# Kernel tuning notes

Hardware: AMD Instinct MI355X
Metric: run time of the kernel (lower is better)

Reference implementation:

```python
import jax, jax.numpy as jnp
import numpy as np

B, L, D = 16, 2048, 320          # batch, frames, stacked feature dim (80 mel * 4 reduction)
CODEBOOK_SIZE, CODEBOOK_DIM = 8192, 16


def setup_inputs() -> dict:
    key = jax.random.key(0)
    k1, k2, k3 = jax.random.split(key, 3)
    masked_target_values = jax.random.normal(k1, (B, L, D), dtype=jnp.float32)
    # xavier_uniform_ for shape (D, codebook_dim): bound = sqrt(6/(fan_in+fan_out))
    bound = np.sqrt(6.0 / (D + CODEBOOK_DIM)).astype(np.float32)
    project_mat = jax.random.uniform(k2, (D, CODEBOOK_DIM), dtype=jnp.float32,
                                     minval=-bound, maxval=bound)
    cb = jax.random.normal(k3, (CODEBOOK_SIZE, CODEBOOK_DIM), dtype=jnp.float32)
    codebook_norm = cb / jnp.maximum(jnp.linalg.norm(cb, axis=-1, keepdims=True), 1e-12)
    return {"masked_target_values": masked_target_values,
            "project_mat": project_mat,
            "codebook_norm": codebook_norm}


def reference(masked_target_values, project_mat, codebook_norm):
    # project: (B, L, D) @ (D, K) -> (B, L, K)
    targets = jnp.einsum('bld,dk->blk', masked_target_values, project_mat)
    # L2 normalize along last dim (torch F.normalize with eps=1e-12)
    targets_norm = targets / jnp.maximum(
        jnp.linalg.norm(targets, axis=-1, keepdims=True), 1e-12)
    x2 = jnp.sum(targets_norm * targets_norm, axis=-1, keepdims=True)      # (B, L, 1)
    c2 = jnp.sum(codebook_norm * codebook_norm, axis=-1)                   # (C,)
    xc = jnp.einsum('blk,ck->blc', targets_norm, codebook_norm)            # (B, L, C)
    d2 = jnp.maximum(x2 + c2[None, None, :] - 2.0 * xc, 0.0)
    vector_distances = jnp.sqrt(d2)
    labels = jnp.argmin(vector_distances, axis=-1)                         # (B, L) int
    return labels
```

## Files before the change

### kernel.cpp

```cpp
#include <hip/hip_runtime.h>
#include <cfloat>

#define TOKENS 32768
#define DIM    320
#define NCODE  8192
#define NSPLIT 8
#define SPAN   (NCODE / NSPLIT)
#define NTILE  (SPAN / 32)
#define CERT_UNITS 32u
#define FBWAVES 2048

typedef __attribute__((ext_vector_type(8)))  short short8;
typedef __attribute__((ext_vector_type(16))) float f32x16;
typedef unsigned short ushort_t;
typedef unsigned int   uint_t;

static __device__ __forceinline__ ushort_t f2bf(float f) {
    uint_t u = __float_as_uint(f);
    u += 0x7fffu + ((u >> 16) & 1u);
    return (ushort_t)(u >> 16);
}
static __device__ __forceinline__ float bf2f(ushort_t h) {
    return __uint_as_float(((uint_t)h) << 16);
}
static __device__ __forceinline__ uint_t pack2(ushort_t a, ushort_t b) {
    return (uint_t)a | ((uint_t)b << 16);
}
static __device__ __forceinline__ uint_t umaxu(uint_t a, uint_t b) { return a > b ? a : b; }
static __device__ __forceinline__ uint_t uminu(uint_t a, uint_t b) { return a < b ? a : b; }

__global__ __launch_bounds__(128) void prep_kernel(
    const float* __restrict__ x,
    const float* __restrict__ P,
    const float* __restrict__ cb,
    float* __restrict__ tn,
    float* __restrict__ x2o,
    float* __restrict__ c2o,
    ushort_t* __restrict__ tnpack,
    ushort_t* __restrict__ cbpack,
    int* __restrict__ cnt)
{
    __shared__ float Ps[DIM * 16];
    int bid = blockIdx.x, tid = threadIdx.x;
    if (bid < TOKENS / 128) {
        const float4* P4 = (const float4*)P;
        float4* Ps4 = (float4*)Ps;
        #pragma unroll
        for (int i = 0; i < 10; ++i) Ps4[tid + i * 128] = P4[tid + i * 128];
        __syncthreads();

        int tok = bid * 128 + tid;
        const float4* xr = (const float4*)(x + (size_t)tok * DIM);
        float acc[16];
        #pragma unroll
        for (int k = 0; k < 16; ++k) acc[k] = 0.f;
        for (int c = 0; c < 10; ++c) {
            float4 xv[8];
            #pragma unroll
            for (int u = 0; u < 8; ++u) xv[u] = xr[c * 8 + u];
            #pragma unroll
            for (int u = 0; u < 8; ++u) {
                float xs[4] = {xv[u].x, xv[u].y, xv[u].z, xv[u].w};
                #pragma unroll
                for (int e = 0; e < 4; ++e) {
                    int d = c * 32 + u * 4 + e;
                    const float4* pr = (const float4*)(Ps + d * 16);
                    float4 p0 = pr[0], p1 = pr[1], p2 = pr[2], p3 = pr[3];
                    float xe = xs[e];
                    acc[0] = fmaf(xe, p0.x, acc[0]);   acc[1] = fmaf(xe, p0.y, acc[1]);
                    acc[2] = fmaf(xe, p0.z, acc[2]);   acc[3] = fmaf(xe, p0.w, acc[3]);
                    acc[4] = fmaf(xe, p1.x, acc[4]);   acc[5] = fmaf(xe, p1.y, acc[5]);
                    acc[6] = fmaf(xe, p1.z, acc[6]);   acc[7] = fmaf(xe, p1.w, acc[7]);
                    acc[8] = fmaf(xe, p2.x, acc[8]);   acc[9] = fmaf(xe, p2.y, acc[9]);
                    acc[10] = fmaf(xe, p2.z, acc[10]); acc[11] = fmaf(xe, p2.w, acc[11]);
                    acc[12] = fmaf(xe, p3.x, acc[12]); acc[13] = fmaf(xe, p3.y, acc[13]);
                    acc[14] = fmaf(xe, p3.z, acc[14]); acc[15] = fmaf(xe, p3.w, acc[15]);
                }
            }
        }
        float ss = 0.f;
        #pragma unroll
        for (int k = 0; k < 16; ++k) ss = fmaf(acc[k], acc[k], ss);
        float nrm = fmaxf(sqrtf(ss), 1e-12f);
        float t[16];
        #pragma unroll
        for (int k = 0; k < 16; ++k) t[k] = acc[k] / nrm;
        float xx = 0.f;
        #pragma unroll
        for (int k = 0; k < 16; ++k) xx = fmaf(t[k], t[k], xx);

        float4* tf = (float4*)(tn + (size_t)tok * 16);
        tf[0] = make_float4(t[0], t[1], t[2], t[3]);
        tf[1] = make_float4(t[4], t[5], t[6], t[7]);
        tf[2] = make_float4(t[8], t[9], t[10], t[11]);
        tf[3] = make_float4(t[12], t[13], t[14], t[15]);
        x2o[tok] = xx;

        ushort_t hi[16], lo[16];
        #pragma unroll
        for (int k = 0; k < 16; ++k) {
            hi[k] = f2bf(t[k]);
            lo[k] = f2bf(t[k] - bf2f(hi[k]));
        }
        uint4* dst = (uint4*)(tnpack + (size_t)tok * 32);
        dst[0] = make_uint4(pack2(hi[0], hi[1]), pack2(hi[2], hi[3]),
                            pack2(hi[4], hi[5]), pack2(hi[6], hi[7]));
        dst[1] = make_uint4(pack2(hi[8], hi[9]), pack2(hi[10], hi[11]),
                            pack2(hi[12], hi[13]), pack2(hi[14], hi[15]));
        dst[2] = make_uint4(pack2(lo[0], lo[1]), pack2(lo[2], lo[3]),
                            pack2(lo[4], lo[5]), pack2(lo[6], lo[7]));
        dst[3] = make_uint4(pack2(lo[8], lo[9]), pack2(lo[10], lo[11]),
                            pack2(lo[12], lo[13]), pack2(lo[14], lo[15]));
    } else {
        int j = (bid - TOKENS / 128) * 128 + tid;
        const float4* cr4 = (const float4*)(cb + (size_t)j * 16);
        float4 c0 = cr4[0], c1 = cr4[1], c2v = cr4[2], c3 = cr4[3];
        float c[16] = {c0.x, c0.y, c0.z, c0.w, c1.x, c1.y, c1.z, c1.w,
                       c2v.x, c2v.y, c2v.z, c2v.w, c3.x, c3.y, c3.z, c3.w};
        float s = 0.f;
        #pragma unroll
        for (int k = 0; k < 16; ++k) s = fmaf(c[k], c[k], s);
        c2o[j] = s;
        ushort_t hi[16], lo[16];
        #pragma unroll
        for (int k = 0; k < 16; ++k) {
            hi[k] = f2bf(c[k]);
            lo[k] = f2bf(c[k] - bf2f(hi[k]));
        }
        uint4* dst = (uint4*)(cbpack + (size_t)j * 32);
        dst[0] = make_uint4(pack2(hi[0], hi[1]), pack2(hi[2], hi[3]),
                            pack2(hi[4], hi[5]), pack2(hi[6], hi[7]));
        dst[1] = make_uint4(pack2(hi[8], hi[9]), pack2(hi[10], hi[11]),
                            pack2(hi[12], hi[13]), pack2(hi[14], hi[15]));
        dst[2] = make_uint4(pack2(lo[0], lo[1]), pack2(lo[2], lo[3]),
                            pack2(lo[4], lo[5]), pack2(lo[6], lo[7]));
        dst[3] = make_uint4(pack2(lo[8], lo[9]), pack2(lo[10], lo[11]),
                            pack2(lo[12], lo[13]), pack2(lo[14], lo[15]));
        if (j == 0) cnt[0] = 0;
    }
}

__global__ __launch_bounds__(256, 4) void search_kernel(
    const ushort_t* __restrict__ tnpack,
    const ushort_t* __restrict__ cbpack,
    uint_t* __restrict__ pp1,
    uint_t* __restrict__ pp2)
{
    int lane = threadIdx.x & 63;
    int wave = threadIdx.x >> 6;
    int half = lane >> 5;
    int l31  = lane & 31;
    int split = blockIdx.y;
    int tbase = blockIdx.x * 128 + wave * 32;

    const ushort_t* tp = tnpack + (size_t)(tbase + l31) * 32;
    short8 hiA = *(const short8*)(tp + half * 8);
    short8 loA = *(const short8*)(tp + 16 + half * 8);

    f32x16 zero = {};
    uint_t p1[16], p2[16];
    #pragma unroll
    for (int r = 0; r < 16; ++r) { p1[r] = 0u; p2[r] = 0u; }

    for (int t = 0; t < NTILE; ++t) {
        int crow = split * SPAN + t * 32 + l31;
        const ushort_t* cp = cbpack + (size_t)crow * 32;
        short8 hiB = *(const short8*)(cp + half * 8);
        short8 loB = *(const short8*)(cp + 16 + half * 8);

        f32x16 acc = __builtin_amdgcn_mfma_f32_32x32x16_bf16(hiA, hiB, zero, 0, 0, 0);
        acc = __builtin_amdgcn_mfma_f32_32x32x16_bf16(loA, hiB, acc, 0, 0, 0);
        acc = __builtin_amdgcn_mfma_f32_32x32x16_bf16(hiA, loB, acc, 0, 0, 0);

        uint_t inv = 8191u - (uint_t)crow;
        #pragma unroll
        for (int r = 0; r < 16; ++r) {
            float kf = fmaf(acc[r], 131072.0f, 131072.0f);
            uint_t ku = (uint_t)kf;
            uint_t p  = (ku << 13) | inv;
            p2[r] = umaxu(p2[r], uminu(p, p1[r]));
            p1[r] = umaxu(p1[r], p);
        }
    }

    #pragma unroll
    for (int mask = 1; mask <= 16; mask <<= 1) {
        #pragma unroll
        for (int r = 0; r < 16; ++r) {
            uint_t a1 = (uint_t)__shfl_xor((int)p1[r], mask);
            uint_t a2 = (uint_t)__shfl_xor((int)p2[r], mask);
            uint_t np2 = umaxu(uminu(p1[r], a1), umaxu(p2[r], a2));
            p1[r] = umaxu(p1[r], a1);
            p2[r] = np2;
        }
    }

    #pragma unroll
    for (int r = 0; r < 16; ++r) {
        if (l31 == r) {
            int mrow = (r & 3) + 8 * (r >> 2) + 4 * half;
            size_t slot = (size_t)split * TOKENS + (tbase + mrow);
            pp1[slot] = p1[r];
            pp2[slot] = p2[r];
        }
    }
}

__global__ __launch_bounds__(256) void reduce_flag_kernel(
    const uint_t* __restrict__ pp1,
    const uint_t* __restrict__ pp2,
    int* __restrict__ out,
    int* __restrict__ cnt,
    int* __restrict__ flag)
{
    int tok = blockIdx.x * 256 + threadIdx.x;
    uint_t p1 = pp1[tok], p2 = pp2[tok];
    #pragma unroll
    for (int s = 1; s < NSPLIT; ++s) {
        uint_t a1 = pp1[(size_t)s * TOKENS + tok];
        uint_t a2 = pp2[(size_t)s * TOKENS + tok];
        uint_t np2 = umaxu(uminu(p1, a1), umaxu(p2, a2));
        p1 = umaxu(p1, a1);
        p2 = np2;
    }
    out[tok] = 8191 - (int)(p1 & 8191u);
    if ((p1 >> 13) - (p2 >> 13) <= CERT_UNITS) {
        int pz = atomicAdd(cnt, 1);
        flag[pz] = tok;
    }
}

__global__ __launch_bounds__(256) void fallback_kernel(
    const float* __restrict__ tn,
    const float* __restrict__ x2i,
    const float* __restrict__ cb,
    const float* __restrict__ c2i,
    const int* __restrict__ cnt,
    const int* __restrict__ flag,
    int* __restrict__ out)
{
    int lane = threadIdx.x & 63;
    int wid = blockIdx.x * 4 + (threadIdx.x >> 6);
    int n = cnt[0];
    for (int f = wid; f < n; f += FBWAVES) {
        int tok = flag[f];
        const float4* tr = (const float4*)(tn + (size_t)tok * 16);
        float4 t0 = tr[0], t1 = tr[1], t2 = tr[2], t3 = tr[3];
        float a[16] = {t0.x, t0.y, t0.z, t0.w, t1.x, t1.y, t1.z, t1.w,
                       t2.x, t2.y, t2.z, t2.w, t3.x, t3.y, t3.z, t3.w};
        float xx = x2i[tok];
        float mn = FLT_MAX;
        int   id = 0x7fffffff;

        int j = lane;
        const float4* c4p = (const float4*)(cb + (size_t)j * 16);
        float4 n0 = c4p[0], n1 = c4p[1], n2 = c4p[2], n3 = c4p[3];
        float ncc = c2i[j];

        for (int jj = 0; jj < 128; ++jj) {
            float4 c0 = n0, c1 = n1, c2v = n2, c3 = n3;
            float cc = ncc;
            int cj = j;
            j += 64;
            if (jj < 127) {
                const float4* nx = (const float4*)(cb + (size_t)j * 16);
                n0 = nx[0]; n1 = nx[1]; n2 = nx[2]; n3 = nx[3];
                ncc = c2i[j];
            }
            float dot = 0.f;
            dot = fmaf(a[0], c0.x, dot);   dot = fmaf(a[1], c0.y, dot);
            dot = fmaf(a[2], c0.z, dot);   dot = fmaf(a[3], c0.w, dot);
            dot = fmaf(a[4], c1.x, dot);   dot = fmaf(a[5], c1.y, dot);
            dot = fmaf(a[6], c1.z, dot);   dot = fmaf(a[7], c1.w, dot);
            dot = fmaf(a[8], c2v.x, dot);  dot = fmaf(a[9], c2v.y, dot);
            dot = fmaf(a[10], c2v.z, dot); dot = fmaf(a[11], c2v.w, dot);
            dot = fmaf(a[12], c3.x, dot);  dot = fmaf(a[13], c3.y, dot);
            dot = fmaf(a[14], c3.z, dot);  dot = fmaf(a[15], c3.w, dot);
            float e = fmaf(-2.f, dot, xx + cc);
            if (e < mn) { mn = e; id = cj; }
        }
        #pragma unroll
        for (int mask = 1; mask <= 32; mask <<= 1) {
            float pmn = __shfl_xor(mn, mask);
            int   pid = __shfl_xor(id, mask);
            bool take = (pmn < mn) || (pmn == mn && pid < id);
            if (take) { mn = pmn; id = pid; }
        }
        if (lane == 0) out[tok] = id;
    }
}

extern "C" void kernel_launch(void* const* d_in, const int* in_sizes, int n_in,
                              void* d_out, int out_size, void* d_ws, size_t ws_size,
                              hipStream_t stream) {
    const float* x   = (const float*)d_in[0];
    const float* P   = (const float*)d_in[1];
    const float* cbn = (const float*)d_in[2];

    float* ws = (float*)d_ws;
    float*  tn   = ws;
    float*  x2   = tn + (size_t)TOKENS * 16;
    float*  c2   = x2 + TOKENS;
    uint_t* pp1  = (uint_t*)(c2 + NCODE);
    uint_t* pp2  = pp1 + (size_t)NSPLIT * TOKENS;
    int*    flag = (int*)(pp2 + (size_t)NSPLIT * TOKENS);
    int*    cnt  = flag + TOKENS;
    ushort_t* tnpack = (ushort_t*)(cnt + 16);
    ushort_t* cbpack = tnpack + (size_t)TOKENS * 32;
    int* labels = (int*)d_out;

    prep_kernel<<<TOKENS / 128 + NCODE / 128, 128, 0, stream>>>(
        x, P, cbn, tn, x2, c2, tnpack, cbpack, cnt);
    dim3 sg(TOKENS / 128, NSPLIT);
    search_kernel<<<sg, 256, 0, stream>>>(tnpack, cbpack, pp1, pp2);
    reduce_flag_kernel<<<TOKENS / 256, 256, 0, stream>>>(pp1, pp2, labels, cnt, flag);
    fallback_kernel<<<FBWAVES / 4, 256, 0, stream>>>(tn, x2, cbn, c2, cnt, flag, labels);
}
```

Before: 185.0 us.

## Split projection across 8 lanes per token with shuffle reduction

The prep kernel's projection now gives each token 8 lanes. Each lane handles a strided subset of the 320 features and reads x at addresses that coalesce across neighbouring lanes, instead of one thread striding a whole 1280-byte row. Partial sums are combined with xor shuffles, the projection matrix in shared memory is padded to 20-float rows to cut bank conflicts, and the output writes are split across the lanes. This is meant to fix poor memory coalescing and low parallelism (previously only 256 token blocks), at the cost of shuffle work and redundant normalization computed in all 8 lanes.

```diff
diff --git a/kernel.cpp b/kernel.cpp
--- a/kernel.cpp
+++ b/kernel.cpp
@@ -9,6 +9,7 @@
 #define NTILE  (SPAN / 32)
 #define CERT_UNITS 32u
 #define FBWAVES 2048
+#define PROW   20
 
 typedef __attribute__((ext_vector_type(8)))  short short8;
 typedef __attribute__((ext_vector_type(16))) float f32x16;
@@ -29,7 +30,7 @@
 static __device__ __forceinline__ uint_t umaxu(uint_t a, uint_t b) { return a > b ? a : b; }
 static __device__ __forceinline__ uint_t uminu(uint_t a, uint_t b) { return a < b ? a : b; }
 
-__global__ __launch_bounds__(128) void prep_kernel(
+__global__ __launch_bounds__(256) void prep_kernel(
     const float* __restrict__ x,
     const float* __restrict__ P,
     const float* __restrict__ cb,
@@ -40,61 +41,56 @@
     ushort_t* __restrict__ cbpack,
     int* __restrict__ cnt)
 {
-    __shared__ float Ps[DIM * 16];
+    __shared__ float Ps[DIM * PROW];
     int bid = blockIdx.x, tid = threadIdx.x;
-    if (bid < TOKENS / 128) {
+    if (bid < TOKENS / 32) {
         const float4* P4 = (const float4*)P;
-        float4* Ps4 = (float4*)Ps;
-        #pragma unroll
-        for (int i = 0; i < 10; ++i) Ps4[tid + i * 128] = P4[tid + i * 128];
+        #pragma unroll
+        for (int i = 0; i < 5; ++i) {
+            int idx = tid + i * 256;
+            int row = idx >> 2, col = idx & 3;
+            *(float4*)(Ps + row * PROW + col * 4) = P4[idx];
+        }
         __syncthreads();
 
-        int tok = bid * 128 + tid;
-        const float4* xr = (const float4*)(x + (size_t)tok * DIM);
+        int sub = tid & 7;
+        int tok = bid * 32 + (tid >> 3);
+        const float* xr = x + (size_t)tok * DIM;
         float acc[16];
         #pragma unroll
         for (int k = 0; k < 16; ++k) acc[k] = 0.f;
-        for (int c = 0; c < 10; ++c) {
-            float4 xv[8];
+
+        for (int i = 0; i < 40; ++i) {
+            int d = i * 8 + sub;
+            float xv = xr[d];
+            const float4* pr = (const float4*)(Ps + d * PROW);
+            float4 p0 = pr[0], p1 = pr[1], p2 = pr[2], p3 = pr[3];
+            acc[0] = fmaf(xv, p0.x, acc[0]);   acc[1] = fmaf(xv, p0.y, acc[1]);
+            acc[2] = fmaf(xv, p0.z, acc[2]);   acc[3] = fmaf(xv, p0.w, acc[3]);
+            acc[4] = fmaf(xv, p1.x, acc[4]);   acc[5] = fmaf(xv, p1.y, acc[5]);
+            acc[6] = fmaf(xv, p1.z, acc[6]);   acc[7] = fmaf(xv, p1.w, acc[7]);
+            acc[8] = fmaf(xv, p2.x, acc[8]);   acc[9] = fmaf(xv, p2.y, acc[9]);
+            acc[10] = fmaf(xv, p2.z, acc[10]); acc[11] = fmaf(xv, p2.w, acc[11]);
+            acc[12] = fmaf(xv, p3.x, acc[12]); acc[13] = fmaf(xv, p3.y, acc[13]);
+            acc[14] = fmaf(xv, p3.z, acc[14]); acc[15] = fmaf(xv, p3.w, acc[15]);
+        }
+        #pragma unroll
+        for (int m = 1; m <= 4; m <<= 1) {
             #pragma unroll
-            for (int u = 0; u < 8; ++u) xv[u] = xr[c * 8 + u];
-            #pragma unroll
-            for (int u = 0; u < 8; ++u) {
-                float xs[4] = {xv[u].x, xv[u].y, xv[u].z, xv[u].w};
-                #pragma unroll
-                for (int e = 0; e < 4; ++e) {
-                    int d = c * 32 + u * 4 + e;
-                    const float4* pr = (const float4*)(Ps + d * 16);
-                    float4 p0 = pr[0], p1 = pr[1], p2 = pr[2], p3 = pr[3];
-                    float xe = xs[e];
-                    acc[0] = fmaf(xe, p0.x, acc[0]);   acc[1] = fmaf(xe, p0.y, acc[1]);
-                    acc[2] = fmaf(xe, p0.z, acc[2]);   acc[3] = fmaf(xe, p0.w, acc[3]);
-                    acc[4] = fmaf(xe, p1.x, acc[4]);   acc[5] = fmaf(xe, p1.y, acc[5]);
-                    acc[6] = fmaf(xe, p1.z, acc[6]);   acc[7] = fmaf(xe, p1.w, acc[7]);
-                    acc[8] = fmaf(xe, p2.x, acc[8]);   acc[9] = fmaf(xe, p2.y, acc[9]);
-                    acc[10] = fmaf(xe, p2.z, acc[10]); acc[11] = fmaf(xe, p2.w, acc[11]);
-                    acc[12] = fmaf(xe, p3.x, acc[12]); acc[13] = fmaf(xe, p3.y, acc[13]);
-                    acc[14] = fmaf(xe, p3.z, acc[14]); acc[15] = fmaf(xe, p3.w, acc[15]);
-                }
-            }
+            for (int k = 0; k < 16; ++k)
+                acc[k] += __shfl_xor(acc[k], m);
         }
         float ss = 0.f;
         #pragma unroll
         for (int k = 0; k < 16; ++k) ss = fmaf(acc[k], acc[k], ss);
         float nrm = fmaxf(sqrtf(ss), 1e-12f);
+        float inv = 1.0f / nrm;
         float t[16];
         #pragma unroll
-        for (int k = 0; k < 16; ++k) t[k] = acc[k] / nrm;
+        for (int k = 0; k < 16; ++k) t[k] = acc[k] * inv;
         float xx = 0.f;
         #pragma unroll
         for (int k = 0; k < 16; ++k) xx = fmaf(t[k], t[k], xx);
-
-        float4* tf = (float4*)(tn + (size_t)tok * 16);
-        tf[0] = make_float4(t[0], t[1], t[2], t[3]);
-        tf[1] = make_float4(t[4], t[5], t[6], t[7]);
-        tf[2] = make_float4(t[8], t[9], t[10], t[11]);
-        tf[3] = make_float4(t[12], t[13], t[14], t[15]);
-        x2o[tok] = xx;
 
         ushort_t hi[16], lo[16];
         #pragma unroll
@@ -102,17 +98,23 @@
             hi[k] = f2bf(t[k]);
             lo[k] = f2bf(t[k] - bf2f(hi[k]));
         }
+        if (sub < 4) {
+            float4* tf = (float4*)(tn + (size_t)tok * 16);
+            tf[sub] = make_float4(t[4 * sub], t[4 * sub + 1],
+                                  t[4 * sub + 2], t[4 * sub + 3]);
+        }
         uint4* dst = (uint4*)(tnpack + (size_t)tok * 32);
-        dst[0] = make_uint4(pack2(hi[0], hi[1]), pack2(hi[2], hi[3]),
-                            pack2(hi[4], hi[5]), pack2(hi[6], hi[7]));
-        dst[1] = make_uint4(pack2(hi[8], hi[9]), pack2(hi[10], hi[11]),
-                            pack2(hi[12], hi[13]), pack2(hi[14], hi[15]));
-        dst[2] = make_uint4(pack2(lo[0], lo[1]), pack2(lo[2], lo[3]),
-                            pack2(lo[4], lo[5]), pack2(lo[6], lo[7]));
-        dst[3] = make_uint4(pack2(lo[8], lo[9]), pack2(lo[10], lo[11]),
-                            pack2(lo[12], lo[13]), pack2(lo[14], lo[15]));
+        if (sub == 4) dst[0] = make_uint4(pack2(hi[0], hi[1]), pack2(hi[2], hi[3]),
+                                          pack2(hi[4], hi[5]), pack2(hi[6], hi[7]));
+        if (sub == 5) dst[1] = make_uint4(pack2(hi[8], hi[9]), pack2(hi[10], hi[11]),
+                                          pack2(hi[12], hi[13]), pack2(hi[14], hi[15]));
+        if (sub == 6) dst[2] = make_uint4(pack2(lo[0], lo[1]), pack2(lo[2], lo[3]),
+                                          pack2(lo[4], lo[5]), pack2(lo[6], lo[7]));
+        if (sub == 7) dst[3] = make_uint4(pack2(lo[8], lo[9]), pack2(lo[10], lo[11]),
+                                          pack2(lo[12], lo[13]), pack2(lo[14], lo[15]));
+        if (sub == 0) x2o[tok] = xx;
     } else {
-        int j = (bid - TOKENS / 128) * 128 + tid;
+        int j = (bid - TOKENS / 32) * 256 + tid;
         const float4* cr4 = (const float4*)(cb + (size_t)j * 16);
         float4 c0 = cr4[0], c1 = cr4[1], c2v = cr4[2], c3 = cr4[3];
         float c[16] = {c0.x, c0.y, c0.z, c0.w, c1.x, c1.y, c1.z, c1.w,
@@ -309,7 +311,7 @@
     ushort_t* cbpack = tnpack + (size_t)TOKENS * 32;
     int* labels = (int*)d_out;
 
-    prep_kernel<<<TOKENS / 128 + NCODE / 128, 128, 0, stream>>>(
+    prep_kernel<<<TOKENS / 32 + NCODE / 256, 256, 0, stream>>>(
         x, P, cbn, tn, x2, c2, tnpack, cbpack, cnt);
     dim3 sg(TOKENS / 128, NSPLIT);
     search_kernel<<<sg, 256, 0, stream>>>(tnpack, cbpack, pp1, pp2);
```

Result: slower. 190.0 us (+2.7%).
